# Kernel optimization log

Measured on AMD Instinct MI355X. Metric: run time of the kernel, lower is better.

## Reference

```python
import jax, jax.numpy as jnp
import numpy as np

N, F_IN = 50000, 128      # nodes, input channels
H, C = 4, 32              # attention heads, out channels per head (concat -> H*C = 128)
E = 800000                # directed edges (before self loops)
NEG_SLOPE = 0.2
EPS = 1e-5                # GraphNorm eps


def setup_inputs() -> dict:
    key = jax.random.key(0)
    ks = jax.random.split(key, 9)
    s = 1.0 / np.sqrt(F_IN)
    return {
        "x": jax.random.normal(ks[0], (N, F_IN), jnp.float32),
        "edge_index": jax.random.randint(ks[1], (2, E), 0, N, jnp.int32),
        "W_l": jax.random.uniform(ks[2], (F_IN, H * C), jnp.float32, -s, s),  # source proj
        "W_r": jax.random.uniform(ks[3], (F_IN, H * C), jnp.float32, -s, s),  # target proj
        "att": jax.random.uniform(ks[4], (H, C), jnp.float32, -s, s),         # GATv2 attention vector a
        "bias": jnp.zeros((H * C,), jnp.float32),
        "gn_weight": jnp.ones((H * C,), jnp.float32),
        "gn_bias": jnp.zeros((H * C,), jnp.float32),
        "gn_mean_scale": jnp.ones((H * C,), jnp.float32),
    }


def _gatv2_graphnorm(x, edge_index, W_l, W_r, att, bias, gn_weight, gn_bias, gn_mean_scale):
    n = x.shape[0]
    # add self loops (add_self_loops=True)
    ar = jnp.arange(n, dtype=edge_index.dtype)
    src = jnp.concatenate([edge_index[0], ar])  # message source j
    dst = jnp.concatenate([edge_index[1], ar])  # message target i

    x_l = (x @ W_l).reshape(n, H, C)  # source-side features
    x_r = (x @ W_r).reshape(n, H, C)  # target-side features

    # GATv2 score: a . LeakyReLU(W_l x_j + W_r x_i), per edge per head  [E+N, H]
    e = jax.nn.leaky_relu(x_l[src] + x_r[dst], NEG_SLOPE)
    score = jnp.einsum("ehc,hc->eh", e, att)

    # softmax over each destination's incoming edges (segment softmax)
    smax = jax.ops.segment_max(score, dst, num_segments=n)
    ex = jnp.exp(score - smax[dst])
    denom = jax.ops.segment_sum(ex, dst, num_segments=n)
    alpha = ex / denom[dst]  # [E+N, H]

    # aggregate messages: out_i = sum_j alpha_ij * (W_l x_j)
    out = jax.ops.segment_sum(alpha[:, :, None] * x_l[src], dst, num_segments=n)
    out = out.reshape(n, H * C) + bias  # concat heads

    # GraphNorm (single graph): per-feature mean/var over all nodes
    mean = out.mean(axis=0)
    centered = out - gn_mean_scale * mean
    var = (centered * centered).mean(axis=0)
    return gn_weight * centered * jax.lax.rsqrt(var + EPS) + gn_bias


def reference(x, edge_index, W_l, W_r, att, bias, gn_weight, gn_bias, gn_mean_scale):
    return _gatv2_graphnorm(x, edge_index, W_l, W_r, att, bias, gn_weight, gn_bias, gn_mean_scale)
```

## Files before the change

kernel.cpp:

```cpp
#include <hip/hip_runtime.h>
#include <hip/hip_bf16.h>
#include <math.h>

#define N_NODES 50000
#define F_IN 128
#define HC 128
#define N_EDGES 800000
#define E_HALF_R (N_EDGES / 2)
#define NEG_SLOPE 0.2f
#define GN_EPS 1e-5f
#define DEG_STRIDE 16
#define CAP 64
#define GB ((N_NODES + 127) / 128)
#define EBR ((E_HALF_R + 511) / 512)
#define FUSED_GRID (GB + EBR)
#define SN_BLOCKS 512
#define SN_SLOTS (SN_BLOCKS * 2)
#define SN_K 49

typedef __attribute__((ext_vector_type(8))) short short8;
typedef __attribute__((ext_vector_type(4))) float floatx4;

__device__ inline ushort f2bf(float f) {
    unsigned u = __float_as_uint(f);
    u += 0x7FFF + ((u >> 16) & 1);
    return (ushort)(u >> 16);
}

__global__ __launch_bounds__(256) void init_k(const float* __restrict__ Wl,
                                              const float* __restrict__ Wr,
                                              ushort* __restrict__ wtl,
                                              ushort* __restrict__ wtr,
                                              int* __restrict__ deg16,
                                              ushort* __restrict__ csrp,
                                              float* __restrict__ gsum,
                                              unsigned* __restrict__ bar) {
    int gid = blockIdx.x * 256 + threadIdx.x;
    if (gid < 16384) {
        int k = gid >> 7, n = gid & 127;
        wtl[n * 128 + k] = f2bf(Wl[gid]);
        wtr[n * 128 + k] = f2bf(Wr[gid]);
    }
    if (gid < 256) gsum[gid] = 0.f;
    if (gid == 0) *bar = 0u;
    if (gid < N_NODES) {
        deg16[gid * DEG_STRIDE] = 1;
        csrp[(size_t)gid * CAP] = (ushort)gid;
    }
}

__global__ __launch_bounds__(512) void eg_k(const int* __restrict__ ei,
                                            int* __restrict__ deg16,
                                            ushort* __restrict__ csrp,
                                            const float* __restrict__ x,
                                            const ushort* __restrict__ wtl,
                                            const ushort* __restrict__ wtr,
                                            ushort* __restrict__ xlb,
                                            ushort* __restrict__ xrb) {
    __shared__ ushort Wt[2][128][136];
    const int bi = blockIdx.x;
    const int tid = threadIdx.x;
    const bool isG = (bi % 3 == 1);

    if (!isG) {
        const int eb = bi - (bi + 1) / 3;
        int gid = eb * 512 + tid;
        if (gid >= E_HALF_R) return;
        {
            int src = ei[gid], dst = ei[N_EDGES + gid];
            int r = atomicAdd(&deg16[dst * DEG_STRIDE], 1);
            if (r < CAP) csrp[(size_t)dst * CAP + r] = (ushort)src;
        }
        {
            int e = gid + E_HALF_R;
            int src = ei[e], dst = ei[N_EDGES + e];
            int r = atomicAdd(&deg16[dst * DEG_STRIDE], 1);
            if (r < CAP) csrp[(size_t)dst * CAP + r] = (ushort)src;
        }
        return;
    }

    const int gb = bi / 3;
#pragma unroll
    for (int i = 0; i < 4; ++i) {
        int idx = i * 512 + tid;
        int n = idx >> 4, k8 = (idx & 15) * 8;
        *(int4*)&Wt[0][n][k8] = *(const int4*)(wtl + n * 128 + k8);
        *(int4*)&Wt[1][n][k8] = *(const int4*)(wtr + n * 128 + k8);
    }
    __syncthreads();

    const int w = tid >> 6, lane = tid & 63;
    const int quad = lane >> 4, l16 = lane & 15;
    const int rbase = gb * 128 + w * 16;
    const int grow = rbase + l16;
    const float* ap = x + (size_t)(grow < N_NODES ? grow : (N_NODES - 1)) * F_IN + quad * 8;

    floatx4 accL[8], accR[8];
#pragma unroll
    for (int nt = 0; nt < 8; ++nt) {
        accL[nt] = (floatx4){0.f, 0.f, 0.f, 0.f};
        accR[nt] = (floatx4){0.f, 0.f, 0.f, 0.f};
    }

#pragma unroll
    for (int ks = 0; ks < 4; ++ks) {
        float4 a0 = *(const float4*)(ap + ks * 32 + 0);
        float4 a1 = *(const float4*)(ap + ks * 32 + 4);
        short8 af;
        af[0] = (short)f2bf(a0.x); af[1] = (short)f2bf(a0.y);
        af[2] = (short)f2bf(a0.z); af[3] = (short)f2bf(a0.w);
        af[4] = (short)f2bf(a1.x); af[5] = (short)f2bf(a1.y);
        af[6] = (short)f2bf(a1.z); af[7] = (short)f2bf(a1.w);
#pragma unroll
        for (int nt = 0; nt < 8; ++nt) {
            short8 bfl = *(const short8*)&Wt[0][nt * 16 + l16][ks * 32 + quad * 8];
            short8 bfr = *(const short8*)&Wt[1][nt * 16 + l16][ks * 32 + quad * 8];
            accL[nt] = __builtin_amdgcn_mfma_f32_16x16x32_bf16(af, bfl, accL[nt], 0, 0, 0);
            accR[nt] = __builtin_amdgcn_mfma_f32_16x16x32_bf16(af, bfr, accR[nt], 0, 0, 0);
        }
    }
#pragma unroll
    for (int r = 0; r < 4; ++r) {
        int gro = rbase + quad * 4 + r;
        if (gro < N_NODES) {
            ushort* opl = xlb + (size_t)gro * HC + l16;
            ushort* opr = xrb + (size_t)gro * HC + l16;
#pragma unroll
            for (int nt = 0; nt < 8; ++nt) {
                opl[nt * 16] = f2bf(accL[nt][r]);
                opr[nt * 16] = f2bf(accR[nt][r]);
            }
        }
    }
}

__global__ __launch_bounds__(256) void attn_k(const ushort* __restrict__ xlb,
                                              const ushort* __restrict__ xrb,
                                              const int* __restrict__ deg16,
                                              const ushort* __restrict__ csrp,
                                              const float* __restrict__ att,
                                              const float* __restrict__ bias,
                                              float* __restrict__ out) {
    const int wid = threadIdx.x >> 6, lane = threadIdx.x & 63;
    const int dst = blockIdx.x * 4 + wid;
    if (dst >= N_NODES) return;
    const int e = lane >> 4, s = lane & 15;
    float xrv[8], av[8];
    {
        int4 xv = *(const int4*)(xrb + (size_t)dst * HC + s * 8);
        xrv[0] = __uint_as_float(((unsigned)xv.x) << 16);
        xrv[1] = __uint_as_float(((unsigned)xv.x) & 0xffff0000u);
        xrv[2] = __uint_as_float(((unsigned)xv.y) << 16);
        xrv[3] = __uint_as_float(((unsigned)xv.y) & 0xffff0000u);
        xrv[4] = __uint_as_float(((unsigned)xv.z) << 16);
        xrv[5] = __uint_as_float(((unsigned)xv.z) & 0xffff0000u);
        xrv[6] = __uint_as_float(((unsigned)xv.w) << 16);
        xrv[7] = __uint_as_float(((unsigned)xv.w) & 0xffff0000u);
        float4 a0 = *(const float4*)(att + s * 8);
        float4 a1 = *(const float4*)(att + s * 8 + 4);
        av[0] = a0.x; av[1] = a0.y; av[2] = a0.z; av[3] = a0.w;
        av[4] = a1.x; av[5] = a1.y; av[6] = a1.z; av[7] = a1.w;
    }
    float l = 0.f;
    float acc[8] = {0.f, 0.f, 0.f, 0.f, 0.f, 0.f, 0.f, 0.f};
    const int nk = min(deg16[dst * DEG_STRIDE], CAP);
    const int sv = (int)csrp[(size_t)dst * CAP + lane];

#define EDGE_STEP(rv, valid)                                                   \
    {                                                                          \
        float f0 = __uint_as_float(((unsigned)(rv).x) << 16);                  \
        float f1 = __uint_as_float(((unsigned)(rv).x) & 0xffff0000u);          \
        float f2 = __uint_as_float(((unsigned)(rv).y) << 16);                  \
        float f3 = __uint_as_float(((unsigned)(rv).y) & 0xffff0000u);          \
        float f4 = __uint_as_float(((unsigned)(rv).z) << 16);                  \
        float f5 = __uint_as_float(((unsigned)(rv).z) & 0xffff0000u);          \
        float f6 = __uint_as_float(((unsigned)(rv).w) << 16);                  \
        float f7 = __uint_as_float(((unsigned)(rv).w) & 0xffff0000u);          \
        float t, part;                                                         \
        t = f0 + xrv[0]; t = t > 0.f ? t : NEG_SLOPE * t; part = av[0] * t;    \
        t = f1 + xrv[1]; t = t > 0.f ? t : NEG_SLOPE * t; part += av[1] * t;   \
        t = f2 + xrv[2]; t = t > 0.f ? t : NEG_SLOPE * t; part += av[2] * t;   \
        t = f3 + xrv[3]; t = t > 0.f ? t : NEG_SLOPE * t; part += av[3] * t;   \
        t = f4 + xrv[4]; t = t > 0.f ? t : NEG_SLOPE * t; part += av[4] * t;   \
        t = f5 + xrv[5]; t = t > 0.f ? t : NEG_SLOPE * t; part += av[5] * t;   \
        t = f6 + xrv[6]; t = t > 0.f ? t : NEG_SLOPE * t; part += av[6] * t;   \
        t = f7 + xrv[7]; t = t > 0.f ? t : NEG_SLOPE * t; part += av[7] * t;   \
        part += __shfl_xor(part, 1, 4);                                        \
        part += __shfl_xor(part, 2, 4);                                        \
        float p = (valid) ? __expf(part) : 0.f;                                \
        l += p;                                                                \
        acc[0] += p * f0; acc[1] += p * f1; acc[2] += p * f2; acc[3] += p * f3;\
        acc[4] += p * f4; acc[5] += p * f5; acc[6] += p * f6; acc[7] += p * f7;\
    }

    int j = 0;
    for (; j + 8 <= nk; j += 8) {
        int s0 = __shfl(sv, j + e, 64);
        int s1 = __shfl(sv, j + 4 + e, 64);
        int4 r0 = *(const int4*)(xlb + (size_t)s0 * HC + s * 8);
        int4 r1 = *(const int4*)(xlb + (size_t)s1 * HC + s * 8);
        EDGE_STEP(r0, true);
        EDGE_STEP(r1, true);
    }
    for (; j < nk; j += 4) {
        int idx = j + e;
        bool valid = idx < nk;
        int s0 = __shfl(sv, valid ? idx : 0, 64);
        int4 r0 = *(const int4*)(xlb + (size_t)s0 * HC + s * 8);
        EDGE_STEP(r0, valid);
    }
#undef EDGE_STEP

    l += __shfl_xor(l, 16, 64);
    l += __shfl_xor(l, 32, 64);
#pragma unroll
    for (int c = 0; c < 8; ++c) {
        acc[c] += __shfl_xor(acc[c], 16, 64);
        acc[c] += __shfl_xor(acc[c], 32, 64);
    }
    if (e == 0) {
        float inv = 1.0f / l;
        float4 b0 = *(const float4*)(bias + s * 8);
        float4 b1 = *(const float4*)(bias + s * 8 + 4);
        float4 o0 = make_float4(acc[0] * inv + b0.x, acc[1] * inv + b0.y,
                                acc[2] * inv + b0.z, acc[3] * inv + b0.w);
        float4 o1 = make_float4(acc[4] * inv + b1.x, acc[5] * inv + b1.y,
                                acc[6] * inv + b1.z, acc[7] * inv + b1.w);
        *(float4*)(out + (size_t)dst * HC + s * 8)     = o0;
        *(float4*)(out + (size_t)dst * HC + s * 8 + 4) = o1;
    }
}

__global__ __launch_bounds__(256) void sn_k(float* __restrict__ out,
                                            float* __restrict__ gsum,
                                            float* __restrict__ gsumsq,
                                            const float* __restrict__ gw,
                                            const float* __restrict__ gb,
                                            const float* __restrict__ gms,
                                            unsigned* __restrict__ bar) {
    const int f = threadIdx.x & 127;
    const int half = threadIdx.x >> 7;
    const int slot = blockIdx.x * 2 + half;
    float v[SN_K];
    float s = 0.f, s2 = 0.f;
#pragma unroll
    for (int k = 0; k < SN_K; ++k) {
        int r = slot + k * SN_SLOTS;
        float t = (r < N_NODES) ? out[(size_t)r * HC + f] : 0.f;
        v[k] = t;
        s += t; s2 += t * t;
    }
    __shared__ float l1[256], l2[256];
    l1[threadIdx.x] = s; l2[threadIdx.x] = s2;
    __syncthreads();
    if (threadIdx.x < 128) {
        atomicAdd(&gsum[f],   l1[threadIdx.x] + l1[threadIdx.x + 128]);
        atomicAdd(&gsumsq[f], l2[threadIdx.x] + l2[threadIdx.x + 128]);
    }
    __threadfence();
    __syncthreads();
    if (threadIdx.x == 0) {
        __hip_atomic_fetch_add(bar, 1u, __ATOMIC_ACQ_REL, __HIP_MEMORY_SCOPE_AGENT);
        while (__hip_atomic_load(bar, __ATOMIC_ACQUIRE, __HIP_MEMORY_SCOPE_AGENT) < SN_BLOCKS) {}
    }
    __syncthreads();

    const float invN = 1.0f / (float)N_NODES;
    float mean = __hip_atomic_load(&gsum[f],   __ATOMIC_RELAXED, __HIP_MEMORY_SCOPE_AGENT) * invN;
    float msq  = __hip_atomic_load(&gsumsq[f], __ATOMIC_RELAXED, __HIP_MEMORY_SCOPE_AGENT) * invN;
    float g = gms[f];
    float var = msq - 2.f * g * mean * mean + g * g * mean * mean;
    float rstd = rsqrtf(var + GN_EPS);
    float a = gw[f] * rstd;
    float b = gb[f] - a * g * mean;
#pragma unroll
    for (int k = 0; k < SN_K; ++k) {
        int r = slot + k * SN_SLOTS;
        if (r < N_NODES) out[(size_t)r * HC + f] = a * v[k] + b;
    }
}

extern "C" void kernel_launch(void* const* d_in, const int* in_sizes, int n_in,
                              void* d_out, int out_size, void* d_ws, size_t ws_size,
                              hipStream_t stream) {
    const float* x    = (const float*)d_in[0];
    const int*   ei   = (const int*)d_in[1];
    const float* Wl   = (const float*)d_in[2];
    const float* Wr   = (const float*)d_in[3];
    const float* att  = (const float*)d_in[4];
    const float* bias = (const float*)d_in[5];
    const float* gw   = (const float*)d_in[6];
    const float* gb   = (const float*)d_in[7];
    const float* gms  = (const float*)d_in[8];
    float* out = (float*)d_out;

    ushort* xlb   = (ushort*)d_ws;
    ushort* xrb   = xlb + (size_t)N_NODES * HC;
    float*  gsum   = (float*)(xrb + (size_t)N_NODES * HC);
    float*  gsumsq = gsum + HC;
    int*    deg16  = (int*)(gsumsq + HC);
    ushort* csrp = (ushort*)(deg16 + (size_t)N_NODES * DEG_STRIDE);
    ushort* wtl  = csrp + (size_t)N_NODES * CAP;
    ushort* wtr  = wtl + 16384;
    unsigned* bar = (unsigned*)(wtr + 16384);

    hipLaunchKernelGGL(init_k, dim3(196), dim3(256), 0, stream,
                       Wl, Wr, wtl, wtr, deg16, csrp, gsum, bar);
    hipLaunchKernelGGL(eg_k, dim3(FUSED_GRID), dim3(512), 0, stream,
                       ei, deg16, csrp, x, wtl, wtr, xlb, xrb);
    hipLaunchKernelGGL(attn_k, dim3(N_NODES / 4), dim3(256), 0, stream,
                       xlb, xrb, deg16, csrp, att, bias, out);
    hipLaunchKernelGGL(sn_k, dim3(SN_BLOCKS), dim3(256), 0, stream,
                       out, gsum, gsumsq, gw, gb, gms, bar);
}
```

Baseline: 238.8 us.

## Split GraphNorm into separate stats and normalize kernels, drop grid barrier

Replaces the single GraphNorm kernel, which held each thread's 49 values in registers and spun on a global atomic barrier, with two kernels. The first accumulates per-feature sums and sums of squares using float4 loads and a shared-memory tree reduction. The second recomputes the affine coefficients and rewrites the output in place with float4 accesses. This removes the spin barrier and the register pressure of the 49-element array, and widens memory accesses. The cost is re-reading the 25 MB output from memory and one extra kernel launch.

```diff
diff --git a/kernel.cpp b/kernel.cpp
--- a/kernel.cpp
+++ b/kernel.cpp
@@ -14,9 +14,8 @@
 #define GB ((N_NODES + 127) / 128)
 #define EBR ((E_HALF_R + 511) / 512)
 #define FUSED_GRID (GB + EBR)
-#define SN_BLOCKS 512
-#define SN_SLOTS (SN_BLOCKS * 2)
-#define SN_K 49
+#define ST_BLOCKS 256
+#define NM_BLOCKS 2048
 
 typedef __attribute__((ext_vector_type(8))) short short8;
 typedef __attribute__((ext_vector_type(4))) float floatx4;
@@ -33,8 +32,7 @@
                                               ushort* __restrict__ wtr,
                                               int* __restrict__ deg16,
                                               ushort* __restrict__ csrp,
-                                              float* __restrict__ gsum,
-                                              unsigned* __restrict__ bar) {
+                                              float* __restrict__ gsum) {
     int gid = blockIdx.x * 256 + threadIdx.x;
     if (gid < 16384) {
         int k = gid >> 7, n = gid & 127;
@@ -42,7 +40,6 @@
         wtr[n * 128 + k] = f2bf(Wr[gid]);
     }
     if (gid < 256) gsum[gid] = 0.f;
-    if (gid == 0) *bar = 0u;
     if (gid < N_NODES) {
         deg16[gid * DEG_STRIDE] = 1;
         csrp[(size_t)gid * CAP] = (ushort)gid;
@@ -232,52 +229,72 @@
     }
 }
 
-__global__ __launch_bounds__(256) void sn_k(float* __restrict__ out,
-                                            float* __restrict__ gsum,
-                                            float* __restrict__ gsumsq,
-                                            const float* __restrict__ gw,
-                                            const float* __restrict__ gb,
-                                            const float* __restrict__ gms,
-                                            unsigned* __restrict__ bar) {
-    const int f = threadIdx.x & 127;
-    const int half = threadIdx.x >> 7;
-    const int slot = blockIdx.x * 2 + half;
-    float v[SN_K];
-    float s = 0.f, s2 = 0.f;
-#pragma unroll
-    for (int k = 0; k < SN_K; ++k) {
-        int r = slot + k * SN_SLOTS;
-        float t = (r < N_NODES) ? out[(size_t)r * HC + f] : 0.f;
-        v[k] = t;
-        s += t; s2 += t * t;
-    }
-    __shared__ float l1[256], l2[256];
-    l1[threadIdx.x] = s; l2[threadIdx.x] = s2;
+__global__ __launch_bounds__(512) void stats_k(const float* __restrict__ out,
+                                               float* __restrict__ gsum,
+                                               float* __restrict__ gsumsq) {
+    const int t = threadIdx.x;
+    const int fg = t & 31;
+    const int rl = t >> 5;
+    float4 s  = make_float4(0.f, 0.f, 0.f, 0.f);
+    float4 s2 = make_float4(0.f, 0.f, 0.f, 0.f);
+    for (int r = blockIdx.x * 16 + rl; r < N_NODES; r += ST_BLOCKS * 16) {
+        float4 v = *(const float4*)(out + (size_t)r * HC + fg * 4);
+        s.x += v.x; s.y += v.y; s.z += v.z; s.w += v.w;
+        s2.x += v.x * v.x; s2.y += v.y * v.y; s2.z += v.z * v.z; s2.w += v.w * v.w;
+    }
+    __shared__ float4 L1[512], L2[512];
+    L1[t] = s; L2[t] = s2;
     __syncthreads();
-    if (threadIdx.x < 128) {
-        atomicAdd(&gsum[f],   l1[threadIdx.x] + l1[threadIdx.x + 128]);
-        atomicAdd(&gsumsq[f], l2[threadIdx.x] + l2[threadIdx.x + 128]);
-    }
-    __threadfence();
-    __syncthreads();
-    if (threadIdx.x == 0) {
-        __hip_atomic_fetch_add(bar, 1u, __ATOMIC_ACQ_REL, __HIP_MEMORY_SCOPE_AGENT);
-        while (__hip_atomic_load(bar, __ATOMIC_ACQUIRE, __HIP_MEMORY_SCOPE_AGENT) < SN_BLOCKS) {}
-    }
-    __syncthreads();
-
+#pragma unroll
+    for (int off = 256; off >= 32; off >>= 1) {
+        if (t < off) {
+            float4 a = L1[t], b = L1[t + off];
+            a.x += b.x; a.y += b.y; a.z += b.z; a.w += b.w; L1[t] = a;
+            float4 c = L2[t], d = L2[t + off];
+            c.x += d.x; c.y += d.y; c.z += d.z; c.w += d.w; L2[t] = c;
+        }
+        __syncthreads();
+    }
+    if (t < 32) {
+        float4 a = L1[t], c = L2[t];
+        atomicAdd(&gsum[t * 4 + 0], a.x); atomicAdd(&gsum[t * 4 + 1], a.y);
+        atomicAdd(&gsum[t * 4 + 2], a.z); atomicAdd(&gsum[t * 4 + 3], a.w);
+        atomicAdd(&gsumsq[t * 4 + 0], c.x); atomicAdd(&gsumsq[t * 4 + 1], c.y);
+        atomicAdd(&gsumsq[t * 4 + 2], c.z); atomicAdd(&gsumsq[t * 4 + 3], c.w);
+    }
+}
+
+__global__ __launch_bounds__(256) void norm_k(float* __restrict__ out,
+                                              const float* __restrict__ gsum,
+                                              const float* __restrict__ gsumsq,
+                                              const float* __restrict__ gw,
+                                              const float* __restrict__ gb,
+                                              const float* __restrict__ gms) {
+    const int t = threadIdx.x;
+    const int fg = t & 31;
+    const int rl = t >> 5;
     const float invN = 1.0f / (float)N_NODES;
-    float mean = __hip_atomic_load(&gsum[f],   __ATOMIC_RELAXED, __HIP_MEMORY_SCOPE_AGENT) * invN;
-    float msq  = __hip_atomic_load(&gsumsq[f], __ATOMIC_RELAXED, __HIP_MEMORY_SCOPE_AGENT) * invN;
-    float g = gms[f];
-    float var = msq - 2.f * g * mean * mean + g * g * mean * mean;
-    float rstd = rsqrtf(var + GN_EPS);
-    float a = gw[f] * rstd;
-    float b = gb[f] - a * g * mean;
-#pragma unroll
-    for (int k = 0; k < SN_K; ++k) {
-        int r = slot + k * SN_SLOTS;
-        if (r < N_NODES) out[(size_t)r * HC + f] = a * v[k] + b;
+    float4 sm = *(const float4*)(gsum + fg * 4);
+    float4 sq = *(const float4*)(gsumsq + fg * 4);
+    float4 gv = *(const float4*)(gms + fg * 4);
+    float4 wv = *(const float4*)(gw + fg * 4);
+    float4 bv = *(const float4*)(gb + fg * 4);
+    float4 a, b;
+#define MKAB(c)                                                                \
+    {                                                                          \
+        float mean = sm.c * invN, msq = sq.c * invN, g = gv.c;                 \
+        float var = msq - 2.f * g * mean * mean + g * g * mean * mean;         \
+        a.c = wv.c * rsqrtf(var + GN_EPS);                                     \
+        b.c = bv.c - a.c * g * mean;                                           \
+    }
+    MKAB(x) MKAB(y) MKAB(z) MKAB(w)
+#undef MKAB
+    for (int r = blockIdx.x * 8 + rl; r < N_NODES; r += NM_BLOCKS * 8) {
+        float* p = out + (size_t)r * HC + fg * 4;
+        float4 v = *(const float4*)p;
+        v.x = a.x * v.x + b.x; v.y = a.y * v.y + b.y;
+        v.z = a.z * v.z + b.z; v.w = a.w * v.w + b.w;
+        *(float4*)p = v;
     }
 }
 
@@ -303,14 +320,15 @@
     ushort* csrp = (ushort*)(deg16 + (size_t)N_NODES * DEG_STRIDE);
     ushort* wtl  = csrp + (size_t)N_NODES * CAP;
     ushort* wtr  = wtl + 16384;
-    unsigned* bar = (unsigned*)(wtr + 16384);
 
     hipLaunchKernelGGL(init_k, dim3(196), dim3(256), 0, stream,
-                       Wl, Wr, wtl, wtr, deg16, csrp, gsum, bar);
+                       Wl, Wr, wtl, wtr, deg16, csrp, gsum);
     hipLaunchKernelGGL(eg_k, dim3(FUSED_GRID), dim3(512), 0, stream,
                        ei, deg16, csrp, x, wtl, wtr, xlb, xrb);
     hipLaunchKernelGGL(attn_k, dim3(N_NODES / 4), dim3(256), 0, stream,
                        xlb, xrb, deg16, csrp, att, bias, out);
-    hipLaunchKernelGGL(sn_k, dim3(SN_BLOCKS), dim3(256), 0, stream,
-                       out, gsum, gsumsq, gw, gb, gms, bar);
-}
+    hipLaunchKernelGGL(stats_k, dim3(ST_BLOCKS), dim3(512), 0, stream,
+                       out, gsum, gsumsq);
+    hipLaunchKernelGGL(norm_k, dim3(NM_BLOCKS), dim3(256), 0, stream,
+                       out, gsum, gsumsq, gw, gb, gms);
+}
```

After: 216.6 us. 1.1x faster.
